# Performance work log

Hardware: AMD Instinct MI355X
Metric: run time of the kernel (lower is better)

Reference implementation:

```python
import jax, jax.numpy as jnp
import numpy as np

B, T, N = 16, 1024, 512

def setup_inputs() -> dict:
    key = jax.random.key(0)
    ks = jax.random.split(key, 6)
    scale = 1.0 / np.sqrt(N)
    x = jax.random.normal(ks[0], (B, T, N), dtype=jnp.float32)
    Wq = jax.random.normal(ks[1], (N, N), dtype=jnp.float32) * scale
    Wk = jax.random.normal(ks[2], (N, N), dtype=jnp.float32) * scale
    Wv = jax.random.normal(ks[3], (N, N), dtype=jnp.float32) * scale
    Wp = jax.random.normal(ks[4], (N, N), dtype=jnp.float32) * scale
    bp = jnp.zeros((N,), dtype=jnp.float32)
    return {"x": x, "Wq": Wq, "Wk": Wk, "Wv": Wv, "Wp": Wp, "bp": bp}

def reference(x, Wq, Wk, Wv, Wp, bp):
    # x: [B, T, N]; conv1d(k=1) over node channels == 'oi,bit->bot' on x^T [B,N,T]
    xt = jnp.swapaxes(x, -1, -2)                     # [B, N, T]
    q = jnp.einsum('oi,bit->bot', Wq, xt)            # [B, N, T]
    k = jnp.einsum('oi,bit->bot', Wk, xt)
    v = jnp.einsum('oi,bit->bot', Wv, xt)
    n = x.shape[-1]
    attn = jnp.einsum('bnt,bmt->bnm', q, k) * (n ** -0.5)  # [B, N, N]
    attn = jax.nn.softmax(attn, axis=-1)
    px = jnp.einsum('bnm,bmt->bnt', attn, v)         # [B, N, T]
    px = jnp.swapaxes(px, -1, -2)                    # [B, T, N]
    out = jnp.einsum('btn,on->bto', px, Wp) + bp     # Linear(N,N)
    return out
```

## Files before the change

kernel.cpp:

```cpp
#include <hip/hip_runtime.h>
#include <stdint.h>

#define BB 16
#define TT 1024
#define NN 512

typedef unsigned short u16;
typedef __bf16 bf16_t;
typedef bf16_t bf16x8 __attribute__((ext_vector_type(8)));
typedef float f32x4 __attribute__((ext_vector_type(4)));

struct alignas(8) U16x4 { u16 x, y, z, w; };
struct alignas(16) F32x4 { float x, y, z, w; };

__device__ __forceinline__ u16 f2bf(float f) {
    union { float f; uint32_t u; } v; v.f = f;
    uint32_t r = v.u + 0x7fffu + ((v.u >> 16) & 1u);
    return (u16)(r >> 16);
}

__device__ __forceinline__ void gload_lds16(const void* g, void* l) {
    __builtin_amdgcn_global_load_lds(
        (const __attribute__((address_space(1))) void*)g,
        (__attribute__((address_space(3))) void*)l, 16, 0, 0);
}

__device__ __forceinline__ void xcd_swizzle(int gx, int gy, int& bx, int& by) {
    const int nwg  = gx * gy;
    const int orig = by * gx + bx;
    const int q = nwg >> 3, r = nwg & 7;
    const int xcd = orig & 7, loc = orig >> 3;
    const int swz = (xcd < r ? xcd * (q + 1) : r * (q + 1) + (xcd - r) * q) + loc;
    bx = swz % gx;
    by = swz / gx;
}

__global__ __launch_bounds__(256)
void cvt_fused(const float* __restrict__ x,
               const float* __restrict__ Wq, const float* __restrict__ Wk,
               const float* __restrict__ Wv, const float* __restrict__ Wp,
               u16* __restrict__ xb, u16* __restrict__ xT, u16* __restrict__ wb)
{
    __shared__ u16 tile[64][70];
    const int i = threadIdx.x;
    if (blockIdx.z < 16) {
        const int b  = blockIdx.z;
        const int t0 = blockIdx.x * 64;
        const int n0 = blockIdx.y * 64;
#pragma unroll
        for (int rep = 0; rep < 4; rep++) {
            const int lin = rep * 256 + i;
            const int r = lin >> 4, c4 = (lin & 15) * 4;
            const long src = ((long)(b * TT + t0 + r)) * NN + n0 + c4;
            F32x4 f = *(const F32x4*)&x[src];
            U16x4 u;
            u.x = f2bf(f.x); u.y = f2bf(f.y); u.z = f2bf(f.z); u.w = f2bf(f.w);
            *(U16x4*)&xb[src] = u;
            tile[r][c4] = u.x; tile[r][c4 + 1] = u.y; tile[r][c4 + 2] = u.z; tile[r][c4 + 3] = u.w;
        }
        __syncthreads();
#pragma unroll
        for (int rep = 0; rep < 4; rep++) {
            const int lin = rep * 256 + i;
            const int n = lin >> 4, t4 = (lin & 15) * 4;
            U16x4 u;
            u.x = tile[t4][n]; u.y = tile[t4 + 1][n]; u.z = tile[t4 + 2][n]; u.w = tile[t4 + 3][n];
            *(U16x4*)&xT[((long)(b * NN + n0 + n)) * TT + t0 + t4] = u;
        }
    } else {
        const int idx = (blockIdx.z - 16) * 128 + blockIdx.y * 16 + blockIdx.x;
        const int w = idx >> 6, wt = idx & 63;
        const int r0 = (wt >> 3) * 64, c0 = (wt & 7) * 64;
        const float* src = (w == 0) ? Wq : (w == 1) ? Wk : (w == 2) ? Wv : Wp;
        u16* dst = wb + w * 262144;
        if (w != 2) {
#pragma unroll
            for (int rep = 0; rep < 4; rep++) {
                const int lin = rep * 256 + i;
                const int r = lin >> 4, c4 = (lin & 15) * 4;
                F32x4 f = *(const F32x4*)&src[(r0 + r) * 512 + c0 + c4];
                U16x4 u;
                u.x = f2bf(f.x); u.y = f2bf(f.y); u.z = f2bf(f.z); u.w = f2bf(f.w);
                *(U16x4*)&dst[(r0 + r) * 512 + c0 + c4] = u;
            }
        } else {
#pragma unroll
            for (int rep = 0; rep < 4; rep++) {
                const int lin = rep * 256 + i;
                const int r = lin >> 4, c4 = (lin & 15) * 4;
                F32x4 f = *(const F32x4*)&src[(r0 + r) * 512 + c0 + c4];
                tile[r][c4]     = f2bf(f.x); tile[r][c4 + 1] = f2bf(f.y);
                tile[r][c4 + 2] = f2bf(f.z); tile[r][c4 + 3] = f2bf(f.w);
            }
            __syncthreads();
#pragma unroll
            for (int rep = 0; rep < 4; rep++) {
                const int lin = rep * 256 + i;
                const int n = lin >> 4, t4 = (lin & 15) * 4;
                U16x4 u;
                u.x = tile[t4][n]; u.y = tile[t4 + 1][n]; u.z = tile[t4 + 2][n]; u.w = tile[t4 + 3][n];
                *(U16x4*)&dst[(c0 + n) * 512 + r0 + t4] = u;
            }
        }
    }
}

template<int MODE>
__global__ __launch_bounds__(256)
void gemm_nt(const u16* __restrict__ Ag, const u16* __restrict__ Bg,
             void* __restrict__ Cg, const float* __restrict__ bias,
             int Nc, int K, int lda, int ldb,
             long sA, long sB, long sC)
{
    const u16* A  = Ag + (long)blockIdx.z * sA;
    const u16* Bt = Bg + (long)blockIdx.z * sB;

    __shared__ u16 As[3][4096];
    __shared__ u16 Bs[3][4096];

    int bx = blockIdx.x, by = blockIdx.y;
    xcd_swizzle(gridDim.x, gridDim.y, bx, by);

    const int tid  = threadIdx.x;
    const int wave = tid >> 6;
    const int lane = tid & 63;
    const int arow0 = by * 128;
    const int brow0 = bx * 128;
    const int wr = (wave >> 1) * 64;
    const int wc = (wave & 1) * 64;

    const int srow = tid >> 2;
    const int sf   = ((srow >> 1) & 3) << 4;
    const int gcol = ((tid & 3) << 4) ^ sf;
    const char* Asrc = (const char*)A  + (long)(arow0 + srow) * lda * 2 + gcol;
    const char* Bsrc = (const char*)Bt + (long)(brow0 + srow) * ldb * 2 + gcol;
    const long rstepA = (long)64 * lda * 2;
    const long rstepB = (long)64 * ldb * 2;

    f32x4 zero = {0.f, 0.f, 0.f, 0.f};
    f32x4 acc[4][4];
#pragma unroll
    for (int i = 0; i < 4; i++)
#pragma unroll
        for (int j = 0; j < 4; j++) acc[i][j] = zero;

    const int kTiles = K >> 5;

    auto stage = [&](int buf, int kt) {
        const long kb = (long)kt * 64;
        char* ad = (char*)As + buf * 8192 + tid * 16;
        char* bd = (char*)Bs + buf * 8192 + tid * 16;
        gload_lds16(Asrc + kb,          ad);
        gload_lds16(Bsrc + kb,          bd);
        gload_lds16(Asrc + rstepA + kb, ad + 4096);
        gload_lds16(Bsrc + rstepB + kb, bd + 4096);
    };

    stage(0, 0);
    stage(1, 1);
    int cur = 0, nxt2 = 2;
    const int kbyte = (lane >> 4) << 4;
    const int rA = lane & 15;

    for (int kt = 0; kt < kTiles; ++kt) {
        if (kt + 2 < kTiles) {
            stage(nxt2, kt + 2);
            asm volatile("s_waitcnt vmcnt(8)" ::: "memory");
        } else if (kt + 1 < kTiles) {
            asm volatile("s_waitcnt vmcnt(4)" ::: "memory");
        } else {
            asm volatile("s_waitcnt vmcnt(0)" ::: "memory");
        }
        __builtin_amdgcn_s_barrier();
        asm volatile("" ::: "memory");

        bf16x8 av[4], bv[4];
        const char* as = (const char*)As + cur * 8192;
        const char* bs = (const char*)Bs + cur * 8192;
#pragma unroll
        for (int m = 0; m < 4; m++) {
            const int row = wr + m * 16 + rA;
            av[m] = *(const bf16x8*)(as + row * 64 + (kbyte ^ (((row >> 1) & 3) << 4)));
        }
#pragma unroll
        for (int n = 0; n < 4; n++) {
            const int row = wc + n * 16 + rA;
            bv[n] = *(const bf16x8*)(bs + row * 64 + (kbyte ^ (((row >> 1) & 3) << 4)));
        }
#pragma unroll
        for (int m = 0; m < 4; m++)
#pragma unroll
            for (int n = 0; n < 4; n++)
                acc[m][n] = __builtin_amdgcn_mfma_f32_16x16x32_bf16(av[m], bv[n], acc[m][n], 0, 0, 0);

        asm volatile("" ::: "memory");
        __builtin_amdgcn_s_barrier();
        cur = (cur == 2) ? 0 : cur + 1;
        nxt2 = (nxt2 == 2) ? 0 : nxt2 + 1;
    }

    const int r0 = (lane >> 4) << 2;
    const int cl = lane & 15;
#pragma unroll
    for (int m = 0; m < 4; m++) {
        const long gm = (long)arow0 + wr + m * 16 + r0;
#pragma unroll
        for (int n = 0; n < 4; n++) {
            const long gn = (long)brow0 + wc + n * 16 + cl;
            if (MODE == 0) {
                u16* O = (u16*)Cg + blockIdx.z * sC;
#pragma unroll
                for (int r = 0; r < 4; r++)
                    O[(gm + r) * Nc + gn] = f2bf(acc[m][n][r]);
            } else {
                float* O = (float*)Cg + blockIdx.z * sC;
                const float bb = (MODE == 3) ? bias[gn] : 0.f;
#pragma unroll
                for (int r = 0; r < 4; r++)
                    O[(gm + r) * Nc + gn] = acc[m][n][r] + bb;
            }
        }
    }
}

__global__ __launch_bounds__(256)
void softmax_rows(float* __restrict__ S)
{
    const long r = blockIdx.x;
    float* row = S + r * 512;
    const int t = threadIdx.x;
    const int lane = t & 63, wave = t >> 6;
    const float scale = 0.04419417382415922f;

    float a = row[t] * scale;
    float b = row[t + 256] * scale;

    float m = fmaxf(a, b);
#pragma unroll
    for (int o = 32; o; o >>= 1) m = fmaxf(m, __shfl_xor(m, o, 64));

    __shared__ float red[8];
    if (lane == 0) red[wave] = m;
    __syncthreads();
    m = fmaxf(fmaxf(red[0], red[1]), fmaxf(red[2], red[3]));

    float e0 = __expf(a - m), e1 = __expf(b - m);
    float s = e0 + e1;
#pragma unroll
    for (int o = 32; o; o >>= 1) s += __shfl_xor(s, o, 64);
    if (lane == 0) red[wave + 4] = s;
    __syncthreads();
    s = red[4] + red[5] + red[6] + red[7];
    const float inv = 1.f / s;

    u16* P = (u16*)row;
    P[t]       = f2bf(e0 * inv);
    P[t + 256] = f2bf(e1 * inv);
}

extern "C" void kernel_launch(void* const* d_in, const int* in_sizes, int n_in,
                              void* d_out, int out_size, void* d_ws, size_t ws_size,
                              hipStream_t stream)
{
    (void)in_sizes; (void)n_in; (void)out_size; (void)ws_size;
    const float* x  = (const float*)d_in[0];
    const float* Wq = (const float*)d_in[1];
    const float* Wk = (const float*)d_in[2];
    const float* Wv = (const float*)d_in[3];
    const float* Wp = (const float*)d_in[4];
    const float* bp = (const float*)d_in[5];
    float* out = (float*)d_out;

    char* ws = (char*)d_ws;
    size_t o = 0;
    auto alloc = [&](size_t bytes) {
        char* p = ws + o;
        o = (o + bytes + 255) & ~(size_t)255;
        return p;
    };
    u16* xb = (u16*)alloc((size_t)BB * TT * NN * 2);
    u16* xT = (u16*)alloc((size_t)BB * NN * TT * 2);
    u16* wb = (u16*)alloc((size_t)4 * NN * NN * 2);
    u16* G  = (u16*)alloc((size_t)BB * NN * NN * 2);
    u16* H  = (u16*)alloc((size_t)BB * NN * NN * 2);
    float* S = (float*)alloc((size_t)BB * NN * NN * 4);
    u16* Rt = (u16*)alloc((size_t)BB * NN * NN * 2);
    u16* Z  = (u16*)alloc((size_t)BB * NN * NN * 2);

    const u16* wqb  = wb;
    const u16* wkb  = wb + 1 * 262144;
    const u16* wvtb = wb + 2 * 262144;
    const u16* wpb  = wb + 3 * 262144;
    const long NSQ = (long)NN * NN;

    cvt_fused<<<dim3(16, 8, 18), dim3(256), 0, stream>>>(x, Wq, Wk, Wv, Wp, xb, xT, wb);

    const dim3 blk(256);

    gemm_nt<0><<<dim3(4, 4, 16), blk, 0, stream>>>(xT, xT, G, nullptr,
        NN, TT, TT, TT, (long)NN * TT, (long)NN * TT, NSQ);

    gemm_nt<0><<<dim3(4, 4, 16), blk, 0, stream>>>(wqb, G, H, nullptr,
        NN, NN, NN, NN, 0, NSQ, NSQ);

    gemm_nt<2><<<dim3(4, 4, 16), blk, 0, stream>>>(H, wkb, S, nullptr,
        NN, NN, NN, NN, NSQ, 0, NSQ);

    softmax_rows<<<dim3(BB * NN), blk, 0, stream>>>(S);

    gemm_nt<0><<<dim3(4, 4, 16), blk, 0, stream>>>(wvtb, (const u16*)S, Rt, nullptr,
        NN, NN, NN, 1024, 0, (long)NN * 1024, NSQ);

    gemm_nt<0><<<dim3(4, 4, 16), blk, 0, stream>>>(wpb, Rt, Z, nullptr,
        NN, NN, NN, NN, 0, NSQ, NSQ);

    gemm_nt<3><<<dim3(4, 8, 16), blk, 0, stream>>>(xb, Z, out, bp,
        NN, NN, NN, NN, (long)TT * NN, NSQ, (long)TT * NN);
}
```

Baseline: 195.3 us.

## Fuse all stages into one persistent kernel with atomic grid barriers

Replaces the eight separate launches (convert, six GEMMs, softmax) with a single persistent kernel of 256 blocks that runs each stage in turn, separated by a software grid barrier built on an atomic counter. The goal is to remove per-launch overhead and the gaps between dependent kernels. In exchange it drops the XCD swizzle, fixes the grid at 256 blocks, so the last GEMM stage runs two tiles per block and the convert stage loops, and it relies on all blocks being co-resident for the spin barrier to avoid deadlock. It also adds a memset launch to reset the counter.

```diff
diff --git a/kernel.cpp b/kernel.cpp
--- a/kernel.cpp
+++ b/kernel.cpp
@@ -25,101 +25,26 @@
         (__attribute__((address_space(3))) void*)l, 16, 0, 0);
 }
 
-__device__ __forceinline__ void xcd_swizzle(int gx, int gy, int& bx, int& by) {
-    const int nwg  = gx * gy;
-    const int orig = by * gx + bx;
-    const int q = nwg >> 3, r = nwg & 7;
-    const int xcd = orig & 7, loc = orig >> 3;
-    const int swz = (xcd < r ? xcd * (q + 1) : r * (q + 1) + (xcd - r) * q) + loc;
-    bx = swz % gx;
-    by = swz / gx;
-}
-
-__global__ __launch_bounds__(256)
-void cvt_fused(const float* __restrict__ x,
-               const float* __restrict__ Wq, const float* __restrict__ Wk,
-               const float* __restrict__ Wv, const float* __restrict__ Wp,
-               u16* __restrict__ xb, u16* __restrict__ xT, u16* __restrict__ wb)
+__device__ __forceinline__ void gbar(unsigned* cnt, unsigned target) {
+    __syncthreads();
+    if (threadIdx.x == 0) {
+        __threadfence();
+        atomicAdd(cnt, 1u);
+        while (atomicAdd(cnt, 0u) < target)
+            __builtin_amdgcn_s_sleep(2);
+        __threadfence();
+    }
+    __syncthreads();
+}
+
+template<int MODE>
+__device__ void dev_gemm(const u16* __restrict__ A, const u16* __restrict__ Bt,
+                         void* __restrict__ C, const float* __restrict__ bias,
+                         int Nc, int K, int lda, int ldb,
+                         int bx, int by, char* smem)
 {
-    __shared__ u16 tile[64][70];
-    const int i = threadIdx.x;
-    if (blockIdx.z < 16) {
-        const int b  = blockIdx.z;
-        const int t0 = blockIdx.x * 64;
-        const int n0 = blockIdx.y * 64;
-#pragma unroll
-        for (int rep = 0; rep < 4; rep++) {
-            const int lin = rep * 256 + i;
-            const int r = lin >> 4, c4 = (lin & 15) * 4;
-            const long src = ((long)(b * TT + t0 + r)) * NN + n0 + c4;
-            F32x4 f = *(const F32x4*)&x[src];
-            U16x4 u;
-            u.x = f2bf(f.x); u.y = f2bf(f.y); u.z = f2bf(f.z); u.w = f2bf(f.w);
-            *(U16x4*)&xb[src] = u;
-            tile[r][c4] = u.x; tile[r][c4 + 1] = u.y; tile[r][c4 + 2] = u.z; tile[r][c4 + 3] = u.w;
-        }
-        __syncthreads();
-#pragma unroll
-        for (int rep = 0; rep < 4; rep++) {
-            const int lin = rep * 256 + i;
-            const int n = lin >> 4, t4 = (lin & 15) * 4;
-            U16x4 u;
-            u.x = tile[t4][n]; u.y = tile[t4 + 1][n]; u.z = tile[t4 + 2][n]; u.w = tile[t4 + 3][n];
-            *(U16x4*)&xT[((long)(b * NN + n0 + n)) * TT + t0 + t4] = u;
-        }
-    } else {
-        const int idx = (blockIdx.z - 16) * 128 + blockIdx.y * 16 + blockIdx.x;
-        const int w = idx >> 6, wt = idx & 63;
-        const int r0 = (wt >> 3) * 64, c0 = (wt & 7) * 64;
-        const float* src = (w == 0) ? Wq : (w == 1) ? Wk : (w == 2) ? Wv : Wp;
-        u16* dst = wb + w * 262144;
-        if (w != 2) {
-#pragma unroll
-            for (int rep = 0; rep < 4; rep++) {
-                const int lin = rep * 256 + i;
-                const int r = lin >> 4, c4 = (lin & 15) * 4;
-                F32x4 f = *(const F32x4*)&src[(r0 + r) * 512 + c0 + c4];
-                U16x4 u;
-                u.x = f2bf(f.x); u.y = f2bf(f.y); u.z = f2bf(f.z); u.w = f2bf(f.w);
-                *(U16x4*)&dst[(r0 + r) * 512 + c0 + c4] = u;
-            }
-        } else {
-#pragma unroll
-            for (int rep = 0; rep < 4; rep++) {
-                const int lin = rep * 256 + i;
-                const int r = lin >> 4, c4 = (lin & 15) * 4;
-                F32x4 f = *(const F32x4*)&src[(r0 + r) * 512 + c0 + c4];
-                tile[r][c4]     = f2bf(f.x); tile[r][c4 + 1] = f2bf(f.y);
-                tile[r][c4 + 2] = f2bf(f.z); tile[r][c4 + 3] = f2bf(f.w);
-            }
-            __syncthreads();
-#pragma unroll
-            for (int rep = 0; rep < 4; rep++) {
-                const int lin = rep * 256 + i;
-                const int n = lin >> 4, t4 = (lin & 15) * 4;
-                U16x4 u;
-                u.x = tile[t4][n]; u.y = tile[t4 + 1][n]; u.z = tile[t4 + 2][n]; u.w = tile[t4 + 3][n];
-                *(U16x4*)&dst[(c0 + n) * 512 + r0 + t4] = u;
-            }
-        }
-    }
-}
-
-template<int MODE>
-__global__ __launch_bounds__(256)
-void gemm_nt(const u16* __restrict__ Ag, const u16* __restrict__ Bg,
-             void* __restrict__ Cg, const float* __restrict__ bias,
-             int Nc, int K, int lda, int ldb,
-             long sA, long sB, long sC)
-{
-    const u16* A  = Ag + (long)blockIdx.z * sA;
-    const u16* Bt = Bg + (long)blockIdx.z * sB;
-
-    __shared__ u16 As[3][4096];
-    __shared__ u16 Bs[3][4096];
-
-    int bx = blockIdx.x, by = blockIdx.y;
-    xcd_swizzle(gridDim.x, gridDim.y, bx, by);
+    char* AsB = smem;
+    char* BsB = smem + 24576;
 
     const int tid  = threadIdx.x;
     const int wave = tid >> 6;
@@ -148,8 +73,8 @@
 
     auto stage = [&](int buf, int kt) {
         const long kb = (long)kt * 64;
-        char* ad = (char*)As + buf * 8192 + tid * 16;
-        char* bd = (char*)Bs + buf * 8192 + tid * 16;
+        char* ad = AsB + buf * 8192 + tid * 16;
+        char* bd = BsB + buf * 8192 + tid * 16;
         gload_lds16(Asrc + kb,          ad);
         gload_lds16(Bsrc + kb,          bd);
         gload_lds16(Asrc + rstepA + kb, ad + 4096);
@@ -175,8 +100,8 @@
         asm volatile("" ::: "memory");
 
         bf16x8 av[4], bv[4];
-        const char* as = (const char*)As + cur * 8192;
-        const char* bs = (const char*)Bs + cur * 8192;
+        const char* as = AsB + cur * 8192;
+        const char* bs = BsB + cur * 8192;
 #pragma unroll
         for (int m = 0; m < 4; m++) {
             const int row = wr + m * 16 + rA;
@@ -195,7 +120,7 @@
 
         asm volatile("" ::: "memory");
         __builtin_amdgcn_s_barrier();
-        cur = (cur == 2) ? 0 : cur + 1;
+        cur  = (cur  == 2) ? 0 : cur  + 1;
         nxt2 = (nxt2 == 2) ? 0 : nxt2 + 1;
     }
 
@@ -208,12 +133,12 @@
         for (int n = 0; n < 4; n++) {
             const long gn = (long)brow0 + wc + n * 16 + cl;
             if (MODE == 0) {
-                u16* O = (u16*)Cg + blockIdx.z * sC;
+                u16* O = (u16*)C;
 #pragma unroll
                 for (int r = 0; r < 4; r++)
                     O[(gm + r) * Nc + gn] = f2bf(acc[m][n][r]);
             } else {
-                float* O = (float*)Cg + blockIdx.z * sC;
+                float* O = (float*)C;
                 const float bb = (MODE == 3) ? bias[gn] : 0.f;
 #pragma unroll
                 for (int r = 0; r < 4; r++)
@@ -224,38 +149,168 @@
 }
 
 __global__ __launch_bounds__(256)
-void softmax_rows(float* __restrict__ S)
+void mega(const float* __restrict__ x,
+          const float* __restrict__ Wq, const float* __restrict__ Wk,
+          const float* __restrict__ Wv, const float* __restrict__ Wp,
+          const float* __restrict__ bp, float* __restrict__ out,
+          u16* xb, u16* xT, u16* wb, u16* G, u16* H, float* S, u16* Rt, u16* Z,
+          unsigned* cnt)
 {
-    const long r = blockIdx.x;
-    float* row = S + r * 512;
-    const int t = threadIdx.x;
-    const int lane = t & 63, wave = t >> 6;
-    const float scale = 0.04419417382415922f;
-
-    float a = row[t] * scale;
-    float b = row[t + 256] * scale;
-
-    float m = fmaxf(a, b);
-#pragma unroll
-    for (int o = 32; o; o >>= 1) m = fmaxf(m, __shfl_xor(m, o, 64));
-
-    __shared__ float red[8];
-    if (lane == 0) red[wave] = m;
-    __syncthreads();
-    m = fmaxf(fmaxf(red[0], red[1]), fmaxf(red[2], red[3]));
-
-    float e0 = __expf(a - m), e1 = __expf(b - m);
-    float s = e0 + e1;
-#pragma unroll
-    for (int o = 32; o; o >>= 1) s += __shfl_xor(s, o, 64);
-    if (lane == 0) red[wave + 4] = s;
-    __syncthreads();
-    s = red[4] + red[5] + red[6] + red[7];
-    const float inv = 1.f / s;
-
-    u16* P = (u16*)row;
-    P[t]       = f2bf(e0 * inv);
-    P[t + 256] = f2bf(e1 * inv);
+    __shared__ __align__(16) char smem[49152];
+
+    const int bid = blockIdx.x;
+    const int i   = threadIdx.x;
+    const long NSQ = (long)NN * NN;
+    unsigned tgt = 0;
+
+    {
+        u16 (*tile)[70] = (u16 (*)[70])smem;
+        for (int u = bid; u < 2304; u += 256) {
+            if (u < 2048) {
+                const int b  = u >> 7;
+                const int t0 = ((u & 127) >> 3) * 64;
+                const int n0 = (u & 7) * 64;
+#pragma unroll
+                for (int rep = 0; rep < 4; rep++) {
+                    const int lin = rep * 256 + i;
+                    const int r = lin >> 4, c4 = (lin & 15) * 4;
+                    const long src = ((long)(b * TT + t0 + r)) * NN + n0 + c4;
+                    F32x4 f = *(const F32x4*)&x[src];
+                    U16x4 u4;
+                    u4.x = f2bf(f.x); u4.y = f2bf(f.y); u4.z = f2bf(f.z); u4.w = f2bf(f.w);
+                    *(U16x4*)&xb[src] = u4;
+                    tile[r][c4] = u4.x; tile[r][c4 + 1] = u4.y;
+                    tile[r][c4 + 2] = u4.z; tile[r][c4 + 3] = u4.w;
+                }
+                __syncthreads();
+#pragma unroll
+                for (int rep = 0; rep < 4; rep++) {
+                    const int lin = rep * 256 + i;
+                    const int n = lin >> 4, t4 = (lin & 15) * 4;
+                    U16x4 u4;
+                    u4.x = tile[t4][n]; u4.y = tile[t4 + 1][n];
+                    u4.z = tile[t4 + 2][n]; u4.w = tile[t4 + 3][n];
+                    *(U16x4*)&xT[((long)(b * NN + n0 + n)) * TT + t0 + t4] = u4;
+                }
+                __syncthreads();
+            } else {
+                const int idx = u - 2048;
+                const int w = idx >> 6, wt = idx & 63;
+                const int r0 = (wt >> 3) * 64, c0 = (wt & 7) * 64;
+                const float* src = (w == 0) ? Wq : (w == 1) ? Wk : (w == 2) ? Wv : Wp;
+                u16* dst = wb + w * 262144;
+                if (w != 2) {
+#pragma unroll
+                    for (int rep = 0; rep < 4; rep++) {
+                        const int lin = rep * 256 + i;
+                        const int r = lin >> 4, c4 = (lin & 15) * 4;
+                        F32x4 f = *(const F32x4*)&src[(r0 + r) * 512 + c0 + c4];
+                        U16x4 u4;
+                        u4.x = f2bf(f.x); u4.y = f2bf(f.y); u4.z = f2bf(f.z); u4.w = f2bf(f.w);
+                        *(U16x4*)&dst[(r0 + r) * 512 + c0 + c4] = u4;
+                    }
+                    __syncthreads(); __syncthreads();
+                } else {
+#pragma unroll
+                    for (int rep = 0; rep < 4; rep++) {
+                        const int lin = rep * 256 + i;
+                        const int r = lin >> 4, c4 = (lin & 15) * 4;
+                        F32x4 f = *(const F32x4*)&src[(r0 + r) * 512 + c0 + c4];
+                        tile[r][c4]     = f2bf(f.x); tile[r][c4 + 1] = f2bf(f.y);
+                        tile[r][c4 + 2] = f2bf(f.z); tile[r][c4 + 3] = f2bf(f.w);
+                    }
+                    __syncthreads();
+#pragma unroll
+                    for (int rep = 0; rep < 4; rep++) {
+                        const int lin = rep * 256 + i;
+                        const int n = lin >> 4, t4 = (lin & 15) * 4;
+                        U16x4 u4;
+                        u4.x = tile[t4][n]; u4.y = tile[t4 + 1][n];
+                        u4.z = tile[t4 + 2][n]; u4.w = tile[t4 + 3][n];
+                        *(U16x4*)&dst[(c0 + n) * 512 + r0 + t4] = u4;
+                    }
+                    __syncthreads();
+                }
+            }
+        }
+    }
+    gbar(cnt, tgt += 256);
+
+    {
+        const int b = bid >> 4, t = bid & 15;
+        dev_gemm<0>(xT + (long)b * NN * TT, xT + (long)b * NN * TT,
+                    G + (long)b * NSQ, nullptr, NN, TT, TT, TT, t & 3, t >> 2, smem);
+    }
+    gbar(cnt, tgt += 256);
+
+    {
+        const int b = bid >> 4, t = bid & 15;
+        dev_gemm<0>(wb, G + (long)b * NSQ,
+                    H + (long)b * NSQ, nullptr, NN, NN, NN, NN, t & 3, t >> 2, smem);
+    }
+    gbar(cnt, tgt += 256);
+
+    {
+        const int b = bid >> 4, t = bid & 15;
+        dev_gemm<2>(H + (long)b * NSQ, wb + 262144,
+                    S + (long)b * NSQ, nullptr, NN, NN, NN, NN, t & 3, t >> 2, smem);
+    }
+    gbar(cnt, tgt += 256);
+
+    {
+        float* red = (float*)smem;
+        const int lane = i & 63, wave = i >> 6;
+        const float scale = 0.04419417382415922f;
+        for (int it = 0; it < 32; ++it) {
+            const long r = (long)bid * 32 + it;
+            float* row = S + r * 512;
+            float a = row[i] * scale;
+            float b = row[i + 256] * scale;
+
+            float m = fmaxf(a, b);
+#pragma unroll
+            for (int o = 32; o; o >>= 1) m = fmaxf(m, __shfl_xor(m, o, 64));
+            if (lane == 0) red[wave] = m;
+            __syncthreads();
+            m = fmaxf(fmaxf(red[0], red[1]), fmaxf(red[2], red[3]));
+
+            float e0 = __expf(a - m), e1 = __expf(b - m);
+            float s = e0 + e1;
+#pragma unroll
+            for (int o = 32; o; o >>= 1) s += __shfl_xor(s, o, 64);
+            if (lane == 0) red[wave + 4] = s;
+            __syncthreads();
+            s = red[4] + red[5] + red[6] + red[7];
+            const float inv = 1.f / s;
+
+            u16* P = (u16*)row;
+            P[i]       = f2bf(e0 * inv);
+            P[i + 256] = f2bf(e1 * inv);
+            __syncthreads();
+        }
+    }
+    gbar(cnt, tgt += 256);
+
+    {
+        const int b = bid >> 4, t = bid & 15;
+        dev_gemm<0>(wb + 2 * 262144, (const u16*)(S + (long)b * NSQ),
+                    Rt + (long)b * NSQ, nullptr, NN, NN, NN, 1024, t & 3, t >> 2, smem);
+    }
+    gbar(cnt, tgt += 256);
+
+    {
+        const int b = bid >> 4, t = bid & 15;
+        dev_gemm<0>(wb + 3 * 262144, Rt + (long)b * NSQ,
+                    Z + (long)b * NSQ, nullptr, NN, NN, NN, NN, t & 3, t >> 2, smem);
+    }
+    gbar(cnt, tgt += 256);
+
+    for (int u = bid; u < 512; u += 256) {
+        const int b = u >> 5, rem = u & 31;
+        dev_gemm<3>(xb + (long)b * TT * NN, Z + (long)b * NSQ,
+                    out + (long)b * TT * NN, bp, NN, NN, NN, NN,
+                    rem & 3, rem >> 2, smem);
+    }
 }
 
 extern "C" void kernel_launch(void* const* d_in, const int* in_sizes, int n_in,
@@ -278,6 +333,7 @@
         o = (o + bytes + 255) & ~(size_t)255;
         return p;
     };
+    unsigned* cnt = (unsigned*)alloc(256);
     u16* xb = (u16*)alloc((size_t)BB * TT * NN * 2);
     u16* xT = (u16*)alloc((size_t)BB * NN * TT * 2);
     u16* wb = (u16*)alloc((size_t)4 * NN * NN * 2);
@@ -287,33 +343,8 @@
     u16* Rt = (u16*)alloc((size_t)BB * NN * NN * 2);
     u16* Z  = (u16*)alloc((size_t)BB * NN * NN * 2);
 
-    const u16* wqb  = wb;
-    const u16* wkb  = wb + 1 * 262144;
-    const u16* wvtb = wb + 2 * 262144;
-    const u16* wpb  = wb + 3 * 262144;
-    const long NSQ = (long)NN * NN;
-
-    cvt_fused<<<dim3(16, 8, 18), dim3(256), 0, stream>>>(x, Wq, Wk, Wv, Wp, xb, xT, wb);
-
-    const dim3 blk(256);
-
-    gemm_nt<0><<<dim3(4, 4, 16), blk, 0, stream>>>(xT, xT, G, nullptr,
-        NN, TT, TT, TT, (long)NN * TT, (long)NN * TT, NSQ);
-
-    gemm_nt<0><<<dim3(4, 4, 16), blk, 0, stream>>>(wqb, G, H, nullptr,
-        NN, NN, NN, NN, 0, NSQ, NSQ);
-
-    gemm_nt<2><<<dim3(4, 4, 16), blk, 0, stream>>>(H, wkb, S, nullptr,
-        NN, NN, NN, NN, NSQ, 0, NSQ);
-
-    softmax_rows<<<dim3(BB * NN), blk, 0, stream>>>(S);
-
-    gemm_nt<0><<<dim3(4, 4, 16), blk, 0, stream>>>(wvtb, (const u16*)S, Rt, nullptr,
-        NN, NN, NN, 1024, 0, (long)NN * 1024, NSQ);
-
-    gemm_nt<0><<<dim3(4, 4, 16), blk, 0, stream>>>(wpb, Rt, Z, nullptr,
-        NN, NN, NN, NN, 0, NSQ, NSQ);
-
-    gemm_nt<3><<<dim3(4, 8, 16), blk, 0, stream>>>(xb, Z, out, bp,
-        NN, NN, NN, NN, (long)TT * NN, NSQ, (long)TT * NN);
-}
+    hipMemsetAsync(cnt, 0, 256, stream);
+    mega<<<dim3(256), dim3(256), 0, stream>>>(
+        x, Wq, Wk, Wv, Wp, bp, out,
+        xb, xT, wb, G, H, S, Rt, Z, cnt);
+}
```

Result: slower. 362.1 us (+85.4%).
